# Performance work log

Hardware: AMD Instinct MI355X
Metric: run time of the kernel (lower is better)

The kernel has to match this reference:

```python
import jax, jax.numpy as jnp
import numpy as np

NUM_HEADS = 4
HEAD_DIM = 64  # out_dim // num_heads = 256 // 4
NEG_SLOPE = 0.2


def setup_inputs() -> dict:
    key = jax.random.key(0)
    k1, k2 = jax.random.split(key)
    h = jax.random.normal(k1, (8, 2048, 256), dtype=jnp.float32)
    # Linear(in_dim, head_dim*num_heads, bias=False): store as [in_dim, out_dim]
    W = jax.random.normal(k2, (256, 256), dtype=jnp.float32) * (1.0 / np.sqrt(256.0))
    return {"h": h, "W": W}


def reference(h, W):
    B, T, _ = h.shape
    # Wh: (B, H, T, D)
    Wh = (h @ W).reshape(B, T, NUM_HEADS, HEAD_DIM).transpose(0, 2, 1, 3)
    scale = 1.0 / (HEAD_DIM ** 0.5)
    # full T x T scores per head, LeakyReLU then softmax over keys
    scores = jnp.einsum('bhtd,bhsd->bhts', Wh, Wh) * scale
    attention = jax.nn.softmax(jax.nn.leaky_relu(scores, negative_slope=NEG_SLOPE), axis=-1)
    h_prime = jnp.einsum('bhts,bhsd->bhtd', attention, Wh)
    # concat=True: (B, T, H*D)
    return h_prime.transpose(0, 2, 1, 3).reshape(B, T, NUM_HEADS * HEAD_DIM)
```

## Files before the change

### kernel.cpp

```cpp
#include <hip/hip_runtime.h>

#define T_SEQ 2048
#define NH 4
#define DH 64

typedef __bf16 bf16x8 __attribute__((ext_vector_type(8)));
typedef float f32x4 __attribute__((ext_vector_type(4)));
typedef unsigned short u16x8 __attribute__((ext_vector_type(8)));

__device__ __forceinline__ unsigned short f2bf_rne(float x) {
  unsigned int u = __builtin_bit_cast(unsigned int, x);
  u += 0x7fffu + ((u >> 16) & 1u);
  return (unsigned short)(u >> 16);
}

__device__ __forceinline__ void async_cp16(const unsigned short* g, unsigned short* l) {
  __builtin_amdgcn_global_load_lds(
      (const __attribute__((address_space(1))) unsigned int*)g,
      (__attribute__((address_space(3))) unsigned int*)l, 16, 0, 0);
}

__global__ __launch_bounds__(256) void wprep(const float* __restrict__ W,
                                             unsigned short* __restrict__ Wt) {
  int tid = blockIdx.x * 256 + threadIdx.x;
  int k = tid >> 8, n = tid & 255;
  float w = W[tid];
  unsigned int u = __builtin_bit_cast(unsigned int, w);
  unsigned short hi = (unsigned short)(u >> 16);
  float fhi = __builtin_bit_cast(float, u & 0xffff0000u);
  float lo = w - fhi;
  Wt[n * 256 + k] = hi;
  Wt[65536 + n * 256 + k] =
      (unsigned short)(__builtin_bit_cast(unsigned int, lo) >> 16);
}

__global__ __launch_bounds__(256, 2) void wh_gemm(
    const float* __restrict__ h, const unsigned short* __restrict__ Wt,
    unsigned short* __restrict__ Kb, unsigned short* __restrict__ Vt) {
  const int tid = threadIdx.x;
  const int wave = tid >> 6;
  const int lane = tid & 63;
  const int l15 = lane & 15;
  const int quad = lane >> 4;
  const int mbase = blockIdx.x * 32;
  const int col0 = wave * 64;

  f32x4 acc[2][4];
#pragma unroll
  for (int mt = 0; mt < 2; mt++)
#pragma unroll
    for (int nt = 0; nt < 4; nt++) acc[mt][nt] = (f32x4){0.f, 0.f, 0.f, 0.f};

  for (int ks = 0; ks < 8; ks++) {
    const int k0 = ks * 32 + quad * 8;
    bf16x8 ahi[2], alo[2];
#pragma unroll
    for (int mt = 0; mt < 2; mt++) {
      const float* hp = h + (size_t)(mbase + mt * 16 + l15) * 256 + k0;
      float xf[8];
      *(float4*)&xf[0] = *(const float4*)hp;
      *(float4*)&xf[4] = *(const float4*)(hp + 4);
      u16x8 hh, ll;
#pragma unroll
      for (int j = 0; j < 8; j++) {
        unsigned int u = __builtin_bit_cast(unsigned int, xf[j]);
        hh[j] = (unsigned short)(u >> 16);
        float lo = xf[j] - __builtin_bit_cast(float, u & 0xffff0000u);
        ll[j] = (unsigned short)(__builtin_bit_cast(unsigned int, lo) >> 16);
      }
      ahi[mt] = __builtin_bit_cast(bf16x8, hh);
      alo[mt] = __builtin_bit_cast(bf16x8, ll);
    }
#pragma unroll
    for (int nt = 0; nt < 4; nt++) {
      const unsigned short* wp = Wt + ((size_t)(col0 + nt * 16 + l15) << 8) + k0;
      bf16x8 bhi = *(const bf16x8*)wp;
      bf16x8 blo = *(const bf16x8*)(wp + 65536);
#pragma unroll
      for (int mt = 0; mt < 2; mt++) {
        acc[mt][nt] = __builtin_amdgcn_mfma_f32_16x16x32_bf16(ahi[mt], bhi, acc[mt][nt], 0, 0, 0);
        acc[mt][nt] = __builtin_amdgcn_mfma_f32_16x16x32_bf16(alo[mt], bhi, acc[mt][nt], 0, 0, 0);
        acc[mt][nt] = __builtin_amdgcn_mfma_f32_16x16x32_bf16(ahi[mt], blo, acc[mt][nt], 0, 0, 0);
      }
    }
  }

  const float s1 = 0.424664717f;
#pragma unroll
  for (int mt = 0; mt < 2; mt++) {
    int row = mbase + mt * 16 + quad * 4;
    int b = row >> 11;
    int tb = row & 2047;
    size_t bh = (size_t)(b * NH + wave);
#pragma unroll
    for (int nt = 0; nt < 4; nt++) {
      int d = nt * 16 + l15;
      ushort4 vp;
#pragma unroll
      for (int r = 0; r < 4; r++) {
        float v = acc[mt][nt][r];
        Kb[(bh * T_SEQ + tb + r) * DH + d] = f2bf_rne(v * s1);
        ((unsigned short*)&vp)[r] = f2bf_rne(v);
      }
      *(ushort4*)&Vt[(bh * DH + d) * T_SEQ + tb] = vp;
    }
  }
}

__global__ __launch_bounds__(256, 4) void attn(
    const unsigned short* __restrict__ Kb, const unsigned short* __restrict__ Vt,
    float* __restrict__ out) {
  __shared__ __align__(16) unsigned short ldsK[2][64 * 64];
  __shared__ __align__(16) unsigned short ldsV[2][64 * 64];
  __shared__ __align__(16) unsigned short ldsP[4][16 * 64];
  const int tid = threadIdx.x;
  const int wave = tid >> 6;
  const int lane = tid & 63;
  const int l15 = lane & 15;
  const int quad = lane >> 4;
  const int lbid = (blockIdx.x & 7) * 128 + (blockIdx.x >> 3);
  const int bh = lbid >> 5;
  const int qtile = lbid & 31;
  const unsigned short* Kbh = Kb + (size_t)bh * T_SEQ * DH;
  const unsigned short* Vbh = Vt + (size_t)bh * DH * T_SEQ;

  const int qrow = qtile * 64 + wave * 16 + l15;
  bf16x8 aq0 = *(const bf16x8*)&Kbh[qrow * DH + quad * 8];
  bf16x8 aq1 = *(const bf16x8*)&Kbh[qrow * DH + 32 + quad * 8];

  f32x4 o[4];
  float lsum[4];
#pragma unroll
  for (int i = 0; i < 4; i++) {
    o[i] = (f32x4){0.f, 0.f, 0.f, 0.f};
    lsum[i] = 0.f;
  }
  unsigned short* Pw = ldsP[wave];

  auto stage = [&](int t, int buf) {
#pragma unroll
    for (int i = 0; i < 2; i++) {
      int slot = i * 256 + tid;
      int r = slot >> 3;
      int c = (slot & 7) ^ (r & 7);
      async_cp16(&Kbh[(t * 64 + r) * DH + c * 8],
                 &ldsK[buf][(i * 256 + wave * 64) * 8]);
      async_cp16(&Vbh[(size_t)r * T_SEQ + t * 64 + c * 8],
                 &ldsV[buf][(i * 256 + wave * 64) * 8]);
    }
  };

  stage(0, 0);

  for (int kt = 0; kt < 32; kt++) {
    const int cur = kt & 1;
    if (kt < 31) {
      stage(kt + 1, cur ^ 1);
      asm volatile("s_waitcnt vmcnt(4)" ::: "memory");
    } else {
      asm volatile("s_waitcnt vmcnt(0)" ::: "memory");
    }
    __builtin_amdgcn_s_barrier();
    __builtin_amdgcn_sched_barrier(0);

    const unsigned short* Kl = ldsK[cur];
    const unsigned short* Vl = ldsV[cur];

    f32x4 sfr[4];
    __builtin_amdgcn_s_setprio(1);
#pragma unroll
    for (int nt = 0; nt < 4; nt++) {
      int key = nt * 16 + l15;
      bf16x8 kf0 = *(const bf16x8*)&Kl[key * 64 + ((quad ^ (key & 7)) << 3)];
      bf16x8 kf1 = *(const bf16x8*)&Kl[key * 64 + (((4 + quad) ^ (key & 7)) << 3)];
      f32x4 s = {0.f, 0.f, 0.f, 0.f};
      s = __builtin_amdgcn_mfma_f32_16x16x32_bf16(aq0, kf0, s, 0, 0, 0);
      s = __builtin_amdgcn_mfma_f32_16x16x32_bf16(aq1, kf1, s, 0, 0, 0);
      sfr[nt] = s;
    }
    __builtin_amdgcn_s_setprio(0);

#pragma unroll
    for (int nt = 0; nt < 4; nt++) {
      int col = nt * 16 + l15;
#pragma unroll
      for (int reg = 0; reg < 4; reg++) {
        float v = sfr[nt][reg];
        float e = __builtin_amdgcn_exp2f(fmaxf(v, 0.2f * v));
        lsum[reg] += e;
        int row = quad * 4 + reg;
        Pw[(row << 6) + (((((col >> 3) ^ (row & 7))) << 3) | (col & 7))] =
            (unsigned short)(__builtin_bit_cast(unsigned int, e) >> 16);
      }
    }
    __builtin_amdgcn_s_waitcnt(0xC07F);

    __builtin_amdgcn_s_setprio(1);
#pragma unroll
    for (int kc = 0; kc < 2; kc++) {
      bf16x8 ap = *(const bf16x8*)&Pw[(l15 << 6) + ((((kc << 2) + quad) ^ (l15 & 7)) << 3)];
#pragma unroll
      for (int nt = 0; nt < 4; nt++) {
        int d = nt * 16 + l15;
        bf16x8 vf = *(const bf16x8*)&Vl[(d << 6) + ((((kc << 2) + quad) ^ (d & 7)) << 3)];
        o[nt] = __builtin_amdgcn_mfma_f32_16x16x32_bf16(ap, vf, o[nt], 0, 0, 0);
      }
    }
    __builtin_amdgcn_s_setprio(0);
    __builtin_amdgcn_sched_barrier(0);
    __builtin_amdgcn_s_barrier();
  }

  float inv[4];
#pragma unroll
  for (int reg = 0; reg < 4; reg++) {
    float l = lsum[reg];
    l += __shfl_xor(l, 1, 64);
    l += __shfl_xor(l, 2, 64);
    l += __shfl_xor(l, 4, 64);
    l += __shfl_xor(l, 8, 64);
    inv[reg] = 1.0f / l;
  }
  const int b = bh >> 2, head = bh & 3;
#pragma unroll
  for (int nt = 0; nt < 4; nt++) {
    int d = nt * 16 + l15;
#pragma unroll
    for (int reg = 0; reg < 4; reg++) {
      int trow = qtile * 64 + wave * 16 + quad * 4 + reg;
      out[((size_t)b * T_SEQ + trow) * 256 + head * 64 + d] = o[nt][reg] * inv[reg];
    }
  }
}

extern "C" void kernel_launch(void* const* d_in, const int* in_sizes, int n_in,
                              void* d_out, int out_size, void* d_ws, size_t ws_size,
                              hipStream_t stream) {
  const float* h = (const float*)d_in[0];
  const float* W = (const float*)d_in[1];
  float* out = (float*)d_out;
  unsigned short* Kb = (unsigned short*)d_ws;
  unsigned short* Vt = Kb + (size_t)32 * T_SEQ * DH;
  unsigned short* Wt = Vt + (size_t)32 * T_SEQ * DH;
  wprep<<<256, 256, 0, stream>>>(W, Wt);
  wh_gemm<<<512, 256, 0, stream>>>(h, Wt, Kb, Vt);
  attn<<<32 * 32, 256, 0, stream>>>(Kb, Vt, out);
}
```

Before: 150.5 us.

## Stage split h tile in LDS and transpose V through LDS in projection GEMM

The projection GEMM now handles 16 rows per block instead of 32 and launches twice as many blocks with higher occupancy bounds. Each block loads the h tile cooperatively once, splits it into bf16 hi/lo parts, and stores them in swizzled LDS, instead of every wave reloading and re-splitting the same rows from global memory. The V transpose goes through a per-wave LDS buffer so the Vt writes become wider contiguous stores. The cost is less reuse of W loads per block and extra LDS traffic. This only touches the small projection stage; the attention kernel, which dominates runtime, is unchanged.

```diff
diff --git a/kernel.cpp b/kernel.cpp
--- a/kernel.cpp
+++ b/kernel.cpp
@@ -26,84 +26,108 @@
   int k = tid >> 8, n = tid & 255;
   float w = W[tid];
   unsigned int u = __builtin_bit_cast(unsigned int, w);
-  unsigned short hi = (unsigned short)(u >> 16);
-  float fhi = __builtin_bit_cast(float, u & 0xffff0000u);
-  float lo = w - fhi;
-  Wt[n * 256 + k] = hi;
+  Wt[n * 256 + k] = (unsigned short)(u >> 16);
+  float lo = w - __builtin_bit_cast(float, u & 0xffff0000u);
   Wt[65536 + n * 256 + k] =
       (unsigned short)(__builtin_bit_cast(unsigned int, lo) >> 16);
 }
 
-__global__ __launch_bounds__(256, 2) void wh_gemm(
+__global__ __launch_bounds__(256, 4) void wh_gemm(
     const float* __restrict__ h, const unsigned short* __restrict__ Wt,
     unsigned short* __restrict__ Kb, unsigned short* __restrict__ Vt) {
+  __shared__ __align__(16) unsigned short Ahi[16 * 256];
+  __shared__ __align__(16) unsigned short Alo[16 * 256];
+  __shared__ __align__(16) unsigned short ldsT[4][64 * 16];
   const int tid = threadIdx.x;
   const int wave = tid >> 6;
   const int lane = tid & 63;
   const int l15 = lane & 15;
   const int quad = lane >> 4;
-  const int mbase = blockIdx.x * 32;
+  const int mbase = blockIdx.x * 16;
   const int col0 = wave * 64;
 
-  f32x4 acc[2][4];
-#pragma unroll
-  for (int mt = 0; mt < 2; mt++)
-#pragma unroll
-    for (int nt = 0; nt < 4; nt++) acc[mt][nt] = (f32x4){0.f, 0.f, 0.f, 0.f};
-
+  {
+    const int r = tid >> 4;
+    const int c16 = tid & 15;
+    const float4* hp = (const float4*)(h + ((size_t)(mbase + r) << 8)) + c16 * 4;
+    float4 f0 = hp[0], f1 = hp[1], f2 = hp[2], f3 = hp[3];
+    u16x8 hi0, lo0, hi1, lo1;
+#define SPLIT1(dsthi, dstlo, idx, v)                                         \
+  {                                                                          \
+    unsigned int u_ = __builtin_bit_cast(unsigned int, (v));                 \
+    dsthi[idx] = (unsigned short)(u_ >> 16);                                 \
+    float r_ = (v) - __builtin_bit_cast(float, u_ & 0xffff0000u);            \
+    dstlo[idx] = (unsigned short)(__builtin_bit_cast(unsigned int, r_) >> 16); \
+  }
+    SPLIT1(hi0, lo0, 0, f0.x) SPLIT1(hi0, lo0, 1, f0.y)
+    SPLIT1(hi0, lo0, 2, f0.z) SPLIT1(hi0, lo0, 3, f0.w)
+    SPLIT1(hi0, lo0, 4, f1.x) SPLIT1(hi0, lo0, 5, f1.y)
+    SPLIT1(hi0, lo0, 6, f1.z) SPLIT1(hi0, lo0, 7, f1.w)
+    SPLIT1(hi1, lo1, 0, f2.x) SPLIT1(hi1, lo1, 1, f2.y)
+    SPLIT1(hi1, lo1, 2, f2.z) SPLIT1(hi1, lo1, 3, f2.w)
+    SPLIT1(hi1, lo1, 4, f3.x) SPLIT1(hi1, lo1, 5, f3.y)
+    SPLIT1(hi1, lo1, 6, f3.z) SPLIT1(hi1, lo1, 7, f3.w)
+#undef SPLIT1
+    const int ch0 = (c16 * 2) ^ (r & 7);
+    const int ch1 = (c16 * 2 + 1) ^ (r & 7);
+    *(u16x8*)&Ahi[r * 256 + ch0 * 8] = hi0;
+    *(u16x8*)&Alo[r * 256 + ch0 * 8] = lo0;
+    *(u16x8*)&Ahi[r * 256 + ch1 * 8] = hi1;
+    *(u16x8*)&Alo[r * 256 + ch1 * 8] = lo1;
+  }
+  __syncthreads();
+
+  f32x4 acc[4];
+#pragma unroll
+  for (int nt = 0; nt < 4; nt++) acc[nt] = (f32x4){0.f, 0.f, 0.f, 0.f};
+
+#pragma unroll 2
   for (int ks = 0; ks < 8; ks++) {
     const int k0 = ks * 32 + quad * 8;
-    bf16x8 ahi[2], alo[2];
-#pragma unroll
-    for (int mt = 0; mt < 2; mt++) {
-      const float* hp = h + (size_t)(mbase + mt * 16 + l15) * 256 + k0;
-      float xf[8];
-      *(float4*)&xf[0] = *(const float4*)hp;
-      *(float4*)&xf[4] = *(const float4*)(hp + 4);
-      u16x8 hh, ll;
-#pragma unroll
-      for (int j = 0; j < 8; j++) {
-        unsigned int u = __builtin_bit_cast(unsigned int, xf[j]);
-        hh[j] = (unsigned short)(u >> 16);
-        float lo = xf[j] - __builtin_bit_cast(float, u & 0xffff0000u);
-        ll[j] = (unsigned short)(__builtin_bit_cast(unsigned int, lo) >> 16);
-      }
-      ahi[mt] = __builtin_bit_cast(bf16x8, hh);
-      alo[mt] = __builtin_bit_cast(bf16x8, ll);
-    }
+    const int ch = (ks * 4 + quad) ^ (l15 & 7);
+    bf16x8 ahi = *(const bf16x8*)&Ahi[l15 * 256 + ch * 8];
+    bf16x8 alo = *(const bf16x8*)&Alo[l15 * 256 + ch * 8];
 #pragma unroll
     for (int nt = 0; nt < 4; nt++) {
       const unsigned short* wp = Wt + ((size_t)(col0 + nt * 16 + l15) << 8) + k0;
       bf16x8 bhi = *(const bf16x8*)wp;
       bf16x8 blo = *(const bf16x8*)(wp + 65536);
-#pragma unroll
-      for (int mt = 0; mt < 2; mt++) {
-        acc[mt][nt] = __builtin_amdgcn_mfma_f32_16x16x32_bf16(ahi[mt], bhi, acc[mt][nt], 0, 0, 0);
-        acc[mt][nt] = __builtin_amdgcn_mfma_f32_16x16x32_bf16(alo[mt], bhi, acc[mt][nt], 0, 0, 0);
-        acc[mt][nt] = __builtin_amdgcn_mfma_f32_16x16x32_bf16(ahi[mt], blo, acc[mt][nt], 0, 0, 0);
-      }
+      acc[nt] = __builtin_amdgcn_mfma_f32_16x16x32_bf16(ahi, bhi, acc[nt], 0, 0, 0);
+      acc[nt] = __builtin_amdgcn_mfma_f32_16x16x32_bf16(alo, bhi, acc[nt], 0, 0, 0);
+      acc[nt] = __builtin_amdgcn_mfma_f32_16x16x32_bf16(ahi, blo, acc[nt], 0, 0, 0);
     }
   }
 
   const float s1 = 0.424664717f;
-#pragma unroll
-  for (int mt = 0; mt < 2; mt++) {
-    int row = mbase + mt * 16 + quad * 4;
-    int b = row >> 11;
-    int tb = row & 2047;
-    size_t bh = (size_t)(b * NH + wave);
-#pragma unroll
-    for (int nt = 0; nt < 4; nt++) {
-      int d = nt * 16 + l15;
-      ushort4 vp;
-#pragma unroll
-      for (int r = 0; r < 4; r++) {
-        float v = acc[mt][nt][r];
-        Kb[(bh * T_SEQ + tb + r) * DH + d] = f2bf_rne(v * s1);
-        ((unsigned short*)&vp)[r] = f2bf_rne(v);
-      }
-      *(ushort4*)&Vt[(bh * DH + d) * T_SEQ + tb] = vp;
-    }
+  const int b = mbase >> 11;
+  const int tb0 = mbase & 2047;
+  const size_t bh = (size_t)(b * NH + wave);
+#pragma unroll
+  for (int nt = 0; nt < 4; nt++) {
+    int d = nt * 16 + l15;
+    int tq = tb0 + quad * 4;
+    Kb[(bh * T_SEQ + tq + 0) * DH + d] = f2bf_rne(acc[nt][0] * s1);
+    Kb[(bh * T_SEQ + tq + 1) * DH + d] = f2bf_rne(acc[nt][1] * s1);
+    Kb[(bh * T_SEQ + tq + 2) * DH + d] = f2bf_rne(acc[nt][2] * s1);
+    Kb[(bh * T_SEQ + tq + 3) * DH + d] = f2bf_rne(acc[nt][3] * s1);
+    ushort4 vp;
+    vp.x = f2bf_rne(acc[nt][0]);
+    vp.y = f2bf_rne(acc[nt][1]);
+    vp.z = f2bf_rne(acc[nt][2]);
+    vp.w = f2bf_rne(acc[nt][3]);
+    *(ushort4*)&ldsT[wave][d * 16 + quad * 4] = vp;
+  }
+  __builtin_amdgcn_s_waitcnt(0xC07F);
+#pragma unroll
+  for (int i = 0; i < 2; i++) {
+    int unit = i * 64 + lane;
+    int d = unit >> 1;
+    int hhalf = unit & 1;
+    ushort4 v0 = *(const ushort4*)&ldsT[wave][d * 16 + hhalf * 8];
+    ushort4 v1 = *(const ushort4*)&ldsT[wave][d * 16 + hhalf * 8 + 4];
+    unsigned short* vb = &Vt[(bh * DH + d) * T_SEQ + tb0 + hhalf * 8];
+    *(ushort4*)vb = v0;
+    *(ushort4*)(vb + 4) = v1;
   }
 }
 
@@ -243,6 +267,6 @@
   unsigned short* Vt = Kb + (size_t)32 * T_SEQ * DH;
   unsigned short* Wt = Vt + (size_t)32 * T_SEQ * DH;
   wprep<<<256, 256, 0, stream>>>(W, Wt);
-  wh_gemm<<<512, 256, 0, stream>>>(h, Wt, Kb, Vt);
+  wh_gemm<<<1024, 256, 0, stream>>>(h, Wt, Kb, Vt);
   attn<<<32 * 32, 256, 0, stream>>>(Kb, Vt, out);
 }
```

Measured after the change: 158.8 us. +5.5%, slower.
